# Kernel tuning notes

Hardware: AMD Instinct MI355X
Metric: run time of the kernel (lower is better)

## Reference

```python
import jax, jax.numpy as jnp
import numpy as np

N, C, NS = 131072, 128, 16
BN_EPS = 1e-5


def setup_inputs() -> dict:
    key = jax.random.key(0)
    ks = jax.random.split(key, 8)
    p = jax.random.normal(ks[0], (N, 3), dtype=jnp.float32)
    u = jax.random.normal(ks[1], (N, C), dtype=jnp.float32)
    o = jnp.array([N], dtype=jnp.int32)  # batch offset (single cloud)
    idx = jax.random.randint(ks[2], (N, NS), 0, N, dtype=jnp.int32)  # precomputed KNN indices
    s = 1.0 / np.sqrt(C)
    W1 = jax.random.uniform(ks[3], (C, C), jnp.float32, -s, s)
    b1 = jax.random.uniform(ks[4], (C,), jnp.float32, -s, s)
    W2 = jax.random.uniform(ks[5], (C, C), jnp.float32, -s, s)
    b2 = jax.random.uniform(ks[6], (C,), jnp.float32, -s, s)
    gamma = jnp.ones((C,), jnp.float32)
    beta = jnp.zeros((C,), jnp.float32)
    return {"p": p, "u": u, "o": o, "idx": idx, "W1": W1, "b1": b1,
            "W2": W2, "b2": b2, "gamma": gamma, "beta": beta}


def reference(p, u, o, idx, W1, b1, W2, b2, gamma, beta):
    # pre_trans: Linear(d_in, d_in)
    u_pre = u @ W1 + b1                                  # [N, C]
    # queryandgroup (use_xyz=False): gather neighbor features by KNN idx
    u_n = u_pre[idx]                                     # [N, NS, C] irregular gather
    # local Laplacian: ReLU(neighbor - center), mean over neighborhood
    lap = jnp.maximum(u_n - u_pre[:, None, :], 0.0).mean(axis=1)  # [N, C]
    # varphi: Linear -> BatchNorm1d (training stats) -> ReLU
    h = lap @ W2 + b2                                    # [N, C]
    mean = h.mean(axis=0)
    var = ((h - mean) ** 2).mean(axis=0)  # biased var, as BN normalization uses
    h = (h - mean) * jax.lax.rsqrt(var + BN_EPS) * gamma + beta
    u_tt = jnp.maximum(h, 0.0)
    return (p, u_tt, o)
```

## Files before the change

kernel.cpp:

```cpp
#include <hip/hip_runtime.h>

#define N_PTS 131072
#define C_DIM 128
#define NS_K  16
#define BN_EPS 1e-5f

typedef unsigned short ushort_t;
typedef unsigned short u16x8 __attribute__((ext_vector_type(8)));
typedef __bf16 bf16x8 __attribute__((ext_vector_type(8)));
typedef float f32x4 __attribute__((ext_vector_type(4)));

__device__ __forceinline__ ushort_t f2b(float f) {
    unsigned int u = __float_as_uint(f);
    u += 0x7FFFu + ((u >> 16) & 1u);
    return (ushort_t)(u >> 16);
}
__device__ __forceinline__ float b2f(ushort_t h) {
    return __uint_as_float((unsigned int)h << 16);
}

__device__ __forceinline__ void acc8(float* lacc, const float* ctr, u16x8 nv) {
    #pragma unroll
    for (int e = 0; e < 8; e++)
        lacc[e] += fmaxf(b2f(nv[e]) - ctr[e], 0.f);
}

__global__ __launch_bounds__(256) void prep_w_kernel(
    const float* __restrict__ W1, const float* __restrict__ W2,
    ushort_t* __restrict__ wT1, ushort_t* __restrict__ wT2)
{
    const int t = blockIdx.x * 256 + threadIdx.x;
    const int n = t & 127;
    const int k = t >> 7;
    wT1[n * 128 + k] = f2b(W1[k * 128 + n]);
    wT2[n * 128 + k] = f2b(W2[k * 128 + n]);
}

template <bool A_BF16, bool STATS>
__global__ __launch_bounds__(256) void gemm_mfma_kernel(
    const void* __restrict__ Aptr, const ushort_t* __restrict__ wT,
    const float* __restrict__ bias, ushort_t* __restrict__ out,
    float* __restrict__ gsum, float* __restrict__ gsq)
{
    __shared__ __align__(16) ushort_t a_sh[128 * 136];
    __shared__ __align__(16) ushort_t w_sh[128 * 136];
    __shared__ float s_sum[128];
    __shared__ float s_sq[128];

    const int tid  = threadIdx.x;
    const int lane = tid & 63;
    const int wv   = tid >> 6;
    const int m16  = lane & 15;
    const int q    = lane >> 4;
    const int base = blockIdx.x * 128;

    if (STATS && tid < 128) { s_sum[tid] = 0.f; s_sq[tid] = 0.f; }

    {
        const int row  = tid >> 1;
        const int half = (tid & 1) * 64;
        ushort_t* as = a_sh + row * 136 + half;
        if (A_BF16) {
            const ushort_t* ag = (const ushort_t*)Aptr + (size_t)(base + row) * 128 + half;
            #pragma unroll
            for (int j = 0; j < 8; j++)
                *(u16x8*)(as + j * 8) = *(const u16x8*)(ag + j * 8);
        } else {
            const float* ag = (const float*)Aptr + (size_t)(base + row) * 128 + half;
            #pragma unroll
            for (int j = 0; j < 8; j++) {
                f32x4 lo = *(const f32x4*)(ag + j * 8);
                f32x4 hi = *(const f32x4*)(ag + j * 8 + 4);
                u16x8 v;
                v[0] = f2b(lo[0]); v[1] = f2b(lo[1]); v[2] = f2b(lo[2]); v[3] = f2b(lo[3]);
                v[4] = f2b(hi[0]); v[5] = f2b(hi[1]); v[6] = f2b(hi[2]); v[7] = f2b(hi[3]);
                *(u16x8*)(as + j * 8) = v;
            }
        }
    }
    {
        const int n    = tid >> 1;
        const int half = (tid & 1) * 64;
        const ushort_t* wg = wT + (size_t)n * 128 + half;
        ushort_t* ws = w_sh + n * 136 + half;
        #pragma unroll
        for (int j = 0; j < 8; j++)
            *(u16x8*)(ws + j * 8) = *(const u16x8*)(wg + j * 8);
    }
    __syncthreads();

    f32x4 acc[2][8];
    #pragma unroll
    for (int i = 0; i < 2; i++)
        #pragma unroll
        for (int c = 0; c < 8; c++) acc[i][c] = (f32x4){0.f, 0.f, 0.f, 0.f};

    const ushort_t* ap0 = a_sh + ((wv * 2 + 0) * 16 + m16) * 136 + q * 8;
    const ushort_t* ap1 = a_sh + ((wv * 2 + 1) * 16 + m16) * 136 + q * 8;
    const ushort_t* wp  = w_sh + m16 * 136 + q * 8;

    #pragma unroll
    for (int k0 = 0; k0 < 128; k0 += 32) {
        bf16x8 a0 = __builtin_bit_cast(bf16x8, *(const u16x8*)(ap0 + k0));
        bf16x8 a1 = __builtin_bit_cast(bf16x8, *(const u16x8*)(ap1 + k0));
        #pragma unroll
        for (int c = 0; c < 8; c++) {
            bf16x8 b = __builtin_bit_cast(bf16x8, *(const u16x8*)(wp + c * (16 * 136) + k0));
            acc[0][c] = __builtin_amdgcn_mfma_f32_16x16x32_bf16(a0, b, acc[0][c], 0, 0, 0);
            acc[1][c] = __builtin_amdgcn_mfma_f32_16x16x32_bf16(a1, b, acc[1][c], 0, 0, 0);
        }
    }

    __syncthreads();

    float psum[8], psq[8];
    #pragma unroll
    for (int c = 0; c < 8; c++) { psum[c] = 0.f; psq[c] = 0.f; }

    #pragma unroll
    for (int c = 0; c < 8; c++) {
        const int col = c * 16 + m16;
        const float bv = bias[col];
        #pragma unroll
        for (int i = 0; i < 2; i++) {
            const int rb = (wv * 2 + i) * 16 + q * 4;
            #pragma unroll
            for (int r = 0; r < 4; r++) {
                const float v = acc[i][c][r] + bv;
                a_sh[(rb + r) * 136 + col] = f2b(v);
                if (STATS) { psum[c] += v; psq[c] += v * v; }
            }
        }
    }
    if (STATS) {
        #pragma unroll
        for (int c = 0; c < 8; c++) {
            atomicAdd(&s_sum[c * 16 + m16], psum[c]);
            atomicAdd(&s_sq[c * 16 + m16],  psq[c]);
        }
    }
    __syncthreads();

    {
        const int r0 = tid >> 4;
        const int c0 = (tid & 15) * 8;
        #pragma unroll
        for (int it = 0; it < 8; it++) {
            const int rl = r0 + it * 16;
            const u16x8 v = *(const u16x8*)(a_sh + rl * 136 + c0);
            *(u16x8*)(out + (size_t)(base + rl) * 128 + c0) = v;
        }
    }
    if (STATS && tid < 128) {
        atomicAdd(&gsum[tid], s_sum[tid]);
        atomicAdd(&gsq[tid],  s_sq[tid]);
    }
}

__global__ __launch_bounds__(256) void lap_gemm_kernel(
    const ushort_t* __restrict__ table, const int* __restrict__ idx,
    const ushort_t* __restrict__ wT, const float* __restrict__ bias,
    ushort_t* __restrict__ out, float* __restrict__ gsum, float* __restrict__ gsq)
{
    __shared__ __align__(16) ushort_t a_sh[128 * 136];
    __shared__ float s_sum[128];
    __shared__ float s_sq[128];

    const int tid  = threadIdx.x;
    const int lane = tid & 63;
    const int wv   = tid >> 6;
    const int m16  = lane & 15;
    const int q    = lane >> 4;
    const int base = blockIdx.x * 128;

    if (tid < 128) { s_sum[tid] = 0.f; s_sq[tid] = 0.f; }

    {
        const int pl = tid >> 4;
        const int c8 = (tid & 15) * 8;
        const ushort_t* tc = table + c8;
        #pragma unroll 1
        for (int it = 0; it < 8; it++) {
            const int pp = it * 16 + pl;
            const size_t prow = (size_t)(base + pp);

            const int4* ig = (const int4*)(idx + prow * NS_K);
            const int4 ia = ig[0];

            const u16x8 cv = *(const u16x8*)(tc + prow * 128);
            float ctr[8];
            #pragma unroll
            for (int e = 0; e < 8; e++) ctr[e] = b2f(cv[e]);
            float lacc[8];
            #pragma unroll
            for (int e = 0; e < 8; e++) lacc[e] = 0.f;

            const u16x8 n0 = *(const u16x8*)(tc + (size_t)ia.x * 128);
            const u16x8 n1 = *(const u16x8*)(tc + (size_t)ia.y * 128);
            const u16x8 n2 = *(const u16x8*)(tc + (size_t)ia.z * 128);
            const u16x8 n3 = *(const u16x8*)(tc + (size_t)ia.w * 128);
            const int4 ib = ig[1];
            acc8(lacc, ctr, n0); acc8(lacc, ctr, n1);
            acc8(lacc, ctr, n2); acc8(lacc, ctr, n3);

            const u16x8 n4 = *(const u16x8*)(tc + (size_t)ib.x * 128);
            const u16x8 n5 = *(const u16x8*)(tc + (size_t)ib.y * 128);
            const u16x8 n6 = *(const u16x8*)(tc + (size_t)ib.z * 128);
            const u16x8 n7 = *(const u16x8*)(tc + (size_t)ib.w * 128);
            const int4 ic = ig[2];
            acc8(lacc, ctr, n4); acc8(lacc, ctr, n5);
            acc8(lacc, ctr, n6); acc8(lacc, ctr, n7);

            const u16x8 m0 = *(const u16x8*)(tc + (size_t)ic.x * 128);
            const u16x8 m1 = *(const u16x8*)(tc + (size_t)ic.y * 128);
            const u16x8 m2 = *(const u16x8*)(tc + (size_t)ic.z * 128);
            const u16x8 m3 = *(const u16x8*)(tc + (size_t)ic.w * 128);
            const int4 id = ig[3];
            acc8(lacc, ctr, m0); acc8(lacc, ctr, m1);
            acc8(lacc, ctr, m2); acc8(lacc, ctr, m3);

            const u16x8 m4 = *(const u16x8*)(tc + (size_t)id.x * 128);
            const u16x8 m5 = *(const u16x8*)(tc + (size_t)id.y * 128);
            const u16x8 m6 = *(const u16x8*)(tc + (size_t)id.z * 128);
            const u16x8 m7 = *(const u16x8*)(tc + (size_t)id.w * 128);
            acc8(lacc, ctr, m4); acc8(lacc, ctr, m5);
            acc8(lacc, ctr, m6); acc8(lacc, ctr, m7);

            u16x8 ov;
            #pragma unroll
            for (int e = 0; e < 8; e++) ov[e] = f2b(lacc[e] * (1.f / (float)NS_K));
            *(u16x8*)(a_sh + pp * 136 + c8) = ov;
        }
    }
    __syncthreads();

    const ushort_t* wp = wT + (size_t)m16 * 128 + q * 8;
    float psum[8], psq[8];
    #pragma unroll
    for (int c = 0; c < 8; c++) { psum[c] = 0.f; psq[c] = 0.f; }

    #pragma unroll 1
    for (int pass = 0; pass < 2; ++pass) {
        const int rt = pass * 4 + wv;

        f32x4 acc[8];
        #pragma unroll
        for (int c = 0; c < 8; c++) acc[c] = (f32x4){0.f, 0.f, 0.f, 0.f};

        const ushort_t* ap = a_sh + (rt * 16 + m16) * 136 + q * 8;
        #pragma unroll
        for (int k0 = 0; k0 < 128; k0 += 32) {
            bf16x8 a0 = __builtin_bit_cast(bf16x8, *(const u16x8*)(ap + k0));
            #pragma unroll
            for (int c = 0; c < 8; c++) {
                bf16x8 b = __builtin_bit_cast(bf16x8, *(const u16x8*)(wp + c * (16 * 128) + k0));
                acc[c] = __builtin_amdgcn_mfma_f32_16x16x32_bf16(a0, b, acc[c], 0, 0, 0);
            }
        }

        #pragma unroll
        for (int c = 0; c < 8; c++) {
            const int col = c * 16 + m16;
            const float bv = bias[col];
            const int rb = rt * 16 + q * 4;
            #pragma unroll
            for (int r = 0; r < 4; r++) {
                const float v = acc[c][r] + bv;
                a_sh[(rb + r) * 136 + col] = f2b(v);
                psum[c] += v; psq[c] += v * v;
            }
        }

        {
            const int r0 = lane >> 4;
            const int c0 = m16 * 8;
            #pragma unroll
            for (int it = 0; it < 4; it++) {
                const int rl = rt * 16 + it * 4 + r0;
                const u16x8 v = *(const u16x8*)(a_sh + rl * 136 + c0);
                *(u16x8*)(out + (size_t)(base + rl) * 128 + c0) = v;
            }
        }
    }

    #pragma unroll
    for (int c = 0; c < 8; c++) {
        atomicAdd(&s_sum[c * 16 + m16], psum[c]);
        atomicAdd(&s_sq[c * 16 + m16],  psq[c]);
    }
    __syncthreads();
    if (tid < 128) {
        atomicAdd(&gsum[tid], s_sum[tid]);
        atomicAdd(&gsq[tid],  s_sq[tid]);
    }
}

__global__ void bn_stats_kernel(const float* __restrict__ gsum,
                                const float* __restrict__ gsq,
                                const float* __restrict__ gamma,
                                const float* __restrict__ beta,
                                float* __restrict__ bnsc, float* __restrict__ bnsh)
{
    const int c = threadIdx.x;
    const float invN = 1.f / (float)N_PTS;
    const float mean = gsum[c] * invN;
    const float var  = gsq[c] * invN - mean * mean;
    const float sc   = rsqrtf(var + BN_EPS) * gamma[c];
    bnsc[c] = sc;
    bnsh[c] = fmaf(-mean, sc, beta[c]);
}

#define BN_BLOCKS ((N_PTS * C_DIM / 8) / 256)
#define P_BLOCKS  ((3 * N_PTS / 4) / 256)

__global__ __launch_bounds__(256) void bn_relu_p_kernel(
    const ushort_t* __restrict__ h, const float* __restrict__ bnsc,
    const float* __restrict__ bnsh, const float* __restrict__ p,
    const int* __restrict__ o, float* __restrict__ out)
{
    const int b = blockIdx.x;
    if (b < BN_BLOCKS) {
        const size_t i = (size_t)b * 256 + threadIdx.x;
        const int c8 = (threadIdx.x * 8) & 127;

        const u16x8 hv = *(const u16x8*)(h + i * 8);
        const f32x4 sc0 = *(const f32x4*)(bnsc + c8);
        const f32x4 sc1 = *(const f32x4*)(bnsc + c8 + 4);
        const f32x4 sh0 = *(const f32x4*)(bnsh + c8);
        const f32x4 sh1 = *(const f32x4*)(bnsh + c8 + 4);

        f32x4 o0, o1;
        #pragma unroll
        for (int e = 0; e < 4; e++) {
            o0[e] = fmaxf(fmaf(b2f(hv[e]),     sc0[e], sh0[e]), 0.f);
            o1[e] = fmaxf(fmaf(b2f(hv[4 + e]), sc1[e], sh1[e]), 0.f);
        }
        float* op = out + (size_t)3 * N_PTS + i * 8;
        *(f32x4*)(op)     = o0;
        *(f32x4*)(op + 4) = o1;
    } else {
        const size_t i = (size_t)(b - BN_BLOCKS) * 256 + threadIdx.x;
        *(f32x4*)(out + i * 4) = *(const f32x4*)(p + i * 4);
        if (i == 0)
            out[(size_t)3 * N_PTS + (size_t)N_PTS * C_DIM] = (float)o[0];
    }
}

extern "C" void kernel_launch(void* const* d_in, const int* in_sizes, int n_in,
                              void* d_out, int out_size, void* d_ws, size_t ws_size,
                              hipStream_t stream) {
    const float* p     = (const float*)d_in[0];
    const float* u     = (const float*)d_in[1];
    const int*   o     = (const int*)d_in[2];
    const int*   idx   = (const int*)d_in[3];
    const float* W1    = (const float*)d_in[4];
    const float* b1    = (const float*)d_in[5];
    const float* W2    = (const float*)d_in[6];
    const float* b2    = (const float*)d_in[7];
    const float* gamma = (const float*)d_in[8];
    const float* beta  = (const float*)d_in[9];
    float* out = (float*)d_out;

    char* ws = (char*)d_ws;
    const size_t buf_bytes = (size_t)N_PTS * C_DIM * sizeof(ushort_t);
    ushort_t* table = (ushort_t*)ws;
    ushort_t* h     = (ushort_t*)(ws + buf_bytes);
    float*    stats = (float*)(ws + 2 * buf_bytes);
    float* gsum = stats;
    float* gsq  = stats + 128;
    float* bnsc = stats + 256;
    float* bnsh = stats + 384;
    ushort_t* wT1 = (ushort_t*)(stats + 512);
    ushort_t* wT2 = wT1 + 128 * 128;

    hipMemsetAsync(stats, 0, 256 * sizeof(float), stream);

    prep_w_kernel<<<64, 256, 0, stream>>>(W1, W2, wT1, wT2);
    gemm_mfma_kernel<false, false><<<N_PTS / 128, 256, 0, stream>>>(
        u, wT1, b1, table, nullptr, nullptr);
    lap_gemm_kernel<<<N_PTS / 128, 256, 0, stream>>>(
        table, idx, wT2, b2, h, gsum, gsq);
    bn_stats_kernel<<<1, 128, 0, stream>>>(gsum, gsq, gamma, beta, bnsc, bnsh);
    bn_relu_p_kernel<<<BN_BLOCKS + P_BLOCKS, 256, 0, stream>>>(
        h, bnsc, bnsh, p, o, out);
}
```

Baseline: 273.9 us.

## Read GEMM weights directly from global memory and split rows into two passes

Drops the shared-memory staging of the transposed weight matrix in the dense GEMM kernel, so the B fragments are read straight from global memory (L2/L1 cached), which halves LDS use per block. Each wave now handles one 16-row tile per pass over two passes with 8 accumulators instead of 16, cutting register pressure. Each wave writes back only its own rows, which drops a block-wide barrier. The aim is higher occupancy and less staging work. The cost is repeated global or cache loads of the weights inside the MFMA loop.

```diff
diff --git a/kernel.cpp b/kernel.cpp
--- a/kernel.cpp
+++ b/kernel.cpp
@@ -43,7 +43,6 @@
     float* __restrict__ gsum, float* __restrict__ gsq)
 {
     __shared__ __align__(16) ushort_t a_sh[128 * 136];
-    __shared__ __align__(16) ushort_t w_sh[128 * 136];
     __shared__ float s_sum[128];
     __shared__ float s_sq[128];
 
@@ -78,82 +77,68 @@
             }
         }
     }
-    {
-        const int n    = tid >> 1;
-        const int half = (tid & 1) * 64;
-        const ushort_t* wg = wT + (size_t)n * 128 + half;
-        ushort_t* ws = w_sh + n * 136 + half;
-        #pragma unroll
-        for (int j = 0; j < 8; j++)
-            *(u16x8*)(ws + j * 8) = *(const u16x8*)(wg + j * 8);
-    }
     __syncthreads();
 
-    f32x4 acc[2][8];
-    #pragma unroll
-    for (int i = 0; i < 2; i++)
-        #pragma unroll
-        for (int c = 0; c < 8; c++) acc[i][c] = (f32x4){0.f, 0.f, 0.f, 0.f};
-
-    const ushort_t* ap0 = a_sh + ((wv * 2 + 0) * 16 + m16) * 136 + q * 8;
-    const ushort_t* ap1 = a_sh + ((wv * 2 + 1) * 16 + m16) * 136 + q * 8;
-    const ushort_t* wp  = w_sh + m16 * 136 + q * 8;
-
-    #pragma unroll
-    for (int k0 = 0; k0 < 128; k0 += 32) {
-        bf16x8 a0 = __builtin_bit_cast(bf16x8, *(const u16x8*)(ap0 + k0));
-        bf16x8 a1 = __builtin_bit_cast(bf16x8, *(const u16x8*)(ap1 + k0));
-        #pragma unroll
-        for (int c = 0; c < 8; c++) {
-            bf16x8 b = __builtin_bit_cast(bf16x8, *(const u16x8*)(wp + c * (16 * 136) + k0));
-            acc[0][c] = __builtin_amdgcn_mfma_f32_16x16x32_bf16(a0, b, acc[0][c], 0, 0, 0);
-            acc[1][c] = __builtin_amdgcn_mfma_f32_16x16x32_bf16(a1, b, acc[1][c], 0, 0, 0);
-        }
-    }
-
-    __syncthreads();
-
+    const ushort_t* wp = wT + (size_t)m16 * 128 + q * 8;
     float psum[8], psq[8];
     #pragma unroll
     for (int c = 0; c < 8; c++) { psum[c] = 0.f; psq[c] = 0.f; }
 
-    #pragma unroll
-    for (int c = 0; c < 8; c++) {
-        const int col = c * 16 + m16;
-        const float bv = bias[col];
-        #pragma unroll
-        for (int i = 0; i < 2; i++) {
-            const int rb = (wv * 2 + i) * 16 + q * 4;
+    #pragma unroll 1
+    for (int pass = 0; pass < 2; ++pass) {
+        const int rt = pass * 4 + wv;
+
+        f32x4 acc[8];
+        #pragma unroll
+        for (int c = 0; c < 8; c++) acc[c] = (f32x4){0.f, 0.f, 0.f, 0.f};
+
+        const ushort_t* ap = a_sh + (rt * 16 + m16) * 136 + q * 8;
+        #pragma unroll
+        for (int k0 = 0; k0 < 128; k0 += 32) {
+            bf16x8 a0 = __builtin_bit_cast(bf16x8, *(const u16x8*)(ap + k0));
+            #pragma unroll
+            for (int c = 0; c < 8; c++) {
+                bf16x8 b = __builtin_bit_cast(bf16x8, *(const u16x8*)(wp + c * (16 * 128) + k0));
+                acc[c] = __builtin_amdgcn_mfma_f32_16x16x32_bf16(a0, b, acc[c], 0, 0, 0);
+            }
+        }
+
+        #pragma unroll
+        for (int c = 0; c < 8; c++) {
+            const int col = c * 16 + m16;
+            const float bv = bias[col];
+            const int rb = rt * 16 + q * 4;
             #pragma unroll
             for (int r = 0; r < 4; r++) {
-                const float v = acc[i][c][r] + bv;
+                const float v = acc[c][r] + bv;
                 a_sh[(rb + r) * 136 + col] = f2b(v);
                 if (STATS) { psum[c] += v; psq[c] += v * v; }
             }
         }
-    }
+
+        {
+            const int r0 = lane >> 4;
+            const int c0 = m16 * 8;
+            #pragma unroll
+            for (int it = 0; it < 4; it++) {
+                const int rl = rt * 16 + it * 4 + r0;
+                const u16x8 v = *(const u16x8*)(a_sh + rl * 136 + c0);
+                *(u16x8*)(out + (size_t)(base + rl) * 128 + c0) = v;
+            }
+        }
+    }
+
     if (STATS) {
         #pragma unroll
         for (int c = 0; c < 8; c++) {
             atomicAdd(&s_sum[c * 16 + m16], psum[c]);
             atomicAdd(&s_sq[c * 16 + m16],  psq[c]);
         }
-    }
-    __syncthreads();
-
-    {
-        const int r0 = tid >> 4;
-        const int c0 = (tid & 15) * 8;
-        #pragma unroll
-        for (int it = 0; it < 8; it++) {
-            const int rl = r0 + it * 16;
-            const u16x8 v = *(const u16x8*)(a_sh + rl * 136 + c0);
-            *(u16x8*)(out + (size_t)(base + rl) * 128 + c0) = v;
-        }
-    }
-    if (STATS && tid < 128) {
-        atomicAdd(&gsum[tid], s_sum[tid]);
-        atomicAdd(&gsq[tid],  s_sq[tid]);
+        __syncthreads();
+        if (tid < 128) {
+            atomicAdd(&gsum[tid], s_sum[tid]);
+            atomicAdd(&gsq[tid],  s_sq[tid]);
+        }
     }
 }
 
```

Measured after the change: 287.3 us. 1.05x slower.
